# Optimization experiments

Measured on AMD Instinct MI355X. Metric: run time of the kernel, lower is better.

## Reference

```python
import jax, jax.numpy as jnp
import numpy as np

E, H, KVH, S, N = 2048, 16, 4, 4096, 1
D = E // H            # head_dim = 128
G = H // KVH          # groups = 4
KV_DIM = KVH * D


def setup_inputs() -> dict:
    key = jax.random.key(0)
    ks = jax.random.split(key, 7)
    sc = 0.02
    seq = jax.random.normal(ks[0], (N, S, E), dtype=jnp.float32)
    # causal mask, 0 = masked (matches masked_fill(mask == 0, -inf))
    mask = jnp.tril(jnp.ones((S, S), dtype=jnp.int32))[None, None]  # [1,1,S,S]
    return {
        "seq": seq,
        "mask": mask,
        "Wq_w": jax.random.normal(ks[1], (E, E), dtype=jnp.float32) * sc,
        "Wq_b": jnp.zeros((E,), dtype=jnp.float32),
        "Wkv_w": jax.random.normal(ks[2], (2 * KV_DIM, E), dtype=jnp.float32) * sc,
        "Wkv_b": jnp.zeros((2 * KV_DIM,), dtype=jnp.float32),
        "Wo_w": jax.random.normal(ks[3], (E, E), dtype=jnp.float32) * sc,
        "Wo_b": jnp.zeros((E,), dtype=jnp.float32),
    }


def reference(seq, mask, Wq_w, Wq_b, Wkv_w, Wkv_b, Wo_w, Wo_b):
    n, s, _ = seq.shape
    q = seq @ Wq_w.T + Wq_b                      # [N,S,E]
    kv = seq @ Wkv_w.T + Wkv_b                   # [N,S,2*KV_DIM]
    Q = q.reshape(n, s, H, D).transpose(0, 2, 1, 3)         # [N,H,S,D]
    KV = kv.reshape(n, s, 2, KVH, D)
    K = KV[:, :, 0].transpose(0, 2, 1, 3)                   # [N,KVH,S,D]
    V = KV[:, :, 1].transpose(0, 2, 1, 3)                   # [N,KVH,S,D]
    # repeat_interleave over head dim (GQA expansion)
    Kr = jnp.repeat(K, G, axis=1)                           # [N,H,S,D]
    Vr = jnp.repeat(V, G, axis=1)
    energy = jnp.einsum("nhqd,nhkd->nhqk", Q, Kr)           # [N,H,S,S]
    neg = jnp.finfo(energy.dtype).min
    energy = jnp.where(mask == 0, neg, energy)
    attn = jax.nn.softmax(energy / jnp.sqrt(jnp.float32(D)), axis=3)
    out = jnp.einsum("nhqk,nhkd->nhqd", attn, Vr)           # [N,H,S,D]
    out = out.transpose(0, 2, 1, 3).reshape(n, s, E)
    out = out @ Wo_w.T + Wo_b
    return out, K, V
```

## Files before the change

kernel.cpp:

```cpp
#include <hip/hip_runtime.h>
#include <cstdint>
#include <cstddef>

typedef __bf16 bf16_t;
typedef __bf16 bf16x4 __attribute__((ext_vector_type(4)));
typedef __bf16 bf16x8 __attribute__((ext_vector_type(8)));
typedef float  f32x4  __attribute__((ext_vector_type(4)));

#define LDQ 3072

__global__ __launch_bounds__(256)
void cast_kernel(const float* __restrict__ in, bf16_t* __restrict__ out, int n8) {
  int i = blockIdx.x * 256 + threadIdx.x;
  if (i >= n8) return;
  const float4* p = reinterpret_cast<const float4*>(in) + (size_t)i * 2;
  float4 a = p[0], b = p[1];
  bf16x8 o;
  o[0] = (bf16_t)a.x; o[1] = (bf16_t)a.y; o[2] = (bf16_t)a.z; o[3] = (bf16_t)a.w;
  o[4] = (bf16_t)b.x; o[5] = (bf16_t)b.y; o[6] = (bf16_t)b.z; o[7] = (bf16_t)b.w;
  *reinterpret_cast<bf16x8*>(out + (size_t)i * 8) = o;
}

template <int MODE>
__global__ __launch_bounds__(256)
void gemm_bt(const bf16_t* __restrict__ A, const bf16_t* __restrict__ B,
             const float* __restrict__ bias0, const float* __restrict__ bias1,
             void* __restrict__ out0, float* __restrict__ kvout,
             bf16_t* __restrict__ vt, int M, int N, int K) {
  __shared__ __align__(16) bf16_t As[128][64];
  __shared__ __align__(16) bf16_t Bs[128][64];
  const int t = threadIdx.x;
  const int l = t & 63, w = t >> 6;
  const int lr = l & 15, lh = l >> 4;
  const int m0 = blockIdx.x * 128, n0 = blockIdx.y * 128;
  const int wm = (w >> 1) * 64, wn = (w & 1) * 64;

  f32x4 acc[4][4] = {};

  for (int kt = 0; kt < K; kt += 64) {
    #pragma unroll
    for (int it = 0; it < 4; ++it) {
      int e = (it * 256 + t) * 8;
      int row = e >> 6, col = e & 63;
      __builtin_amdgcn_global_load_lds(
          (const __attribute__((address_space(1))) void*)(A + (size_t)(m0 + row) * K + kt + col),
          (__attribute__((address_space(3))) void*)(&As[row][col]), 16, 0, 0);
      __builtin_amdgcn_global_load_lds(
          (const __attribute__((address_space(1))) void*)(B + (size_t)(n0 + row) * K + kt + col),
          (__attribute__((address_space(3))) void*)(&Bs[row][col]), 16, 0, 0);
    }
    __syncthreads();
    #pragma unroll
    for (int ks = 0; ks < 2; ++ks) {
      bf16x8 a[4], b[4];
      #pragma unroll
      for (int i = 0; i < 4; ++i)
        a[i] = *reinterpret_cast<const bf16x8*>(&As[wm + i * 16 + lr][ks * 32 + lh * 8]);
      #pragma unroll
      for (int j = 0; j < 4; ++j)
        b[j] = *reinterpret_cast<const bf16x8*>(&Bs[wn + j * 16 + lr][ks * 32 + lh * 8]);
      #pragma unroll
      for (int i = 0; i < 4; ++i)
        #pragma unroll
        for (int j = 0; j < 4; ++j)
          acc[i][j] = __builtin_amdgcn_mfma_f32_16x16x32_bf16(a[i], b[j], acc[i][j], 0, 0, 0);
    }
    __syncthreads();
  }

  #pragma unroll
  for (int j = 0; j < 4; ++j) {
    const int col = n0 + wn + j * 16 + lr;
    float bv;
    if constexpr (MODE == 0) bv = bias0[col];
    else bv = (col < 2048) ? bias0[col] : bias1[col - 2048];
    #pragma unroll
    for (int i = 0; i < 4; ++i) {
      #pragma unroll
      for (int r = 0; r < 4; ++r) {
        const int row = m0 + wm + i * 16 + lh * 4 + r;
        float v = acc[i][j][r] + bv;
        if constexpr (MODE == 0) {
          reinterpret_cast<float*>(out0)[(size_t)row * N + col] = v;
        } else {
          float qv = (col < 2048) ? v * 0.1275187541f : v;
          reinterpret_cast<bf16_t*>(out0)[(size_t)row * N + col] = (bf16_t)qv;
          if (col >= 2048) {
            const int local = col - 2048;
            const int which = local >> 9;
            const int hd    = local & 511;
            kvout[(size_t)which * 2097152 +
                  ((size_t)(hd >> 7) * 4096 + row) * 128 + (hd & 127)] = v;
            if (local >= 512) {
              const int c2 = local - 512;
              vt[(size_t)(c2 >> 7) * 524288 + (size_t)(c2 & 127) * 4096 + row] = (bf16_t)v;
            }
          }
        }
      }
    }
  }
}

__global__ __launch_bounds__(512, 2)
void attn_kernel(const bf16_t* __restrict__ QKVb, const bf16_t* __restrict__ Vt,
                 bf16_t* __restrict__ Ob) {
  __shared__ __align__(16) char smem[65536];
  const int t = threadIdx.x;
  const int w = t >> 6, l = t & 63;
  const int lr = l & 15, lh = l >> 4;
  const int g = w >> 2;
  const int wq = w & 3;
  const int h = blockIdx.y, kvh = h >> 2;

  const char* Kg = (const char*)(QKVb + 2048 + (size_t)kvh * 128);
  const char* Vg = (const char*)(Vt + (size_t)kvh * 524288);

#define STAGE_K(buf, kv0)                                                          \
  {                                                                                \
    _Pragma("unroll")                                                              \
    for (int p = 0; p < 2; ++p) {                                                  \
      int chunk = p * 512 + t;                                                     \
      int row = chunk >> 4, cb = (chunk & 15) << 4;                                \
      __builtin_amdgcn_global_load_lds(                                            \
        (const __attribute__((address_space(1))) void*)                            \
            (Kg + (size_t)((kv0) + row) * 6144 + (cb ^ ((row & 7) << 4))),         \
        (__attribute__((address_space(3))) void*)(smem + (buf) * 16384 + chunk * 16),\
        16, 0, 0);                                                                 \
    }                                                                              \
  }
#define STAGE_V(buf, kv0)                                                          \
  {                                                                                \
    _Pragma("unroll")                                                              \
    for (int p = 0; p < 2; ++p) {                                                  \
      int chunk = p * 512 + t;                                                     \
      int row = chunk >> 3, cb = (chunk & 7) << 4;                                 \
      __builtin_amdgcn_global_load_lds(                                            \
        (const __attribute__((address_space(1))) void*)                            \
            (Vg + (size_t)row * 8192 + (size_t)(kv0) * 2 + (cb ^ ((row & 7) << 4))),\
        (__attribute__((address_space(3))) void*)(smem + 32768 + (buf) * 16384 + chunk * 16),\
        16, 0, 0);                                                                 \
    }                                                                              \
  }

  bf16x8 onesf;
  #pragma unroll
  for (int j = 0; j < 8; ++j) onesf[j] = (bf16_t)1.0f;

  for (int ph = 0; ph < 2; ++ph) {
    const int xt = ph ? 31 - (int)blockIdx.x : (int)blockIdx.x;
    const int q0b = xt * 128;
    const int q0w = q0b + wq * 32;
    const int nIter = 2 * xt + 2;

    bf16x8 qf[2][4];
    #pragma unroll
    for (int sub = 0; sub < 2; ++sub) {
      const bf16_t* qp = QKVb + (size_t)(q0w + sub * 16 + lr) * LDQ + h * 128 + lh * 8;
      #pragma unroll
      for (int kc = 0; kc < 4; ++kc) qf[sub][kc] = *reinterpret_cast<const bf16x8*>(qp + kc * 32);
    }
    __builtin_amdgcn_sched_barrier(0);
    STAGE_K(0, 0);
    STAGE_V(0, 0);
    __builtin_amdgcn_sched_barrier(0);
    STAGE_K(1, 64);
    STAGE_V(1, 64);
    __builtin_amdgcn_sched_barrier(0);

    f32x4 oacc[2][8] = {};
    f32x4 lacc[2] = {};

    auto body = [&](int it, bool masked) {
      const int cur = it & 1;
      const int kv0 = it * 64;
      if (it + 1 < nIter) { asm volatile("s_waitcnt vmcnt(4)" ::: "memory"); }
      else                { asm volatile("s_waitcnt vmcnt(0)" ::: "memory"); }
      __builtin_amdgcn_s_barrier();
      __builtin_amdgcn_sched_barrier(0);

      const char* kb = smem + cur * 16384;
      f32x4 s[2][2] = {};
      __builtin_amdgcn_s_setprio(1);
      #pragma unroll
      for (int n2 = 0; n2 < 2; ++n2) {
        const int row = g * 32 + n2 * 16 + lr;
        const int sw = (row & 7) << 4;
        #pragma unroll
        for (int kc = 0; kc < 4; ++kc) {
          bf16x8 kf = *reinterpret_cast<const bf16x8*>(kb + row * 256 + ((kc * 64 + lh * 16) ^ sw));
          s[0][n2] = __builtin_amdgcn_mfma_f32_16x16x32_bf16(kf, qf[0][kc], s[0][n2], 0, 0, 0);
          s[1][n2] = __builtin_amdgcn_mfma_f32_16x16x32_bf16(kf, qf[1][kc], s[1][n2], 0, 0, 0);
        }
      }
      __builtin_amdgcn_s_setprio(0);

      bf16x8 pa[2];
      #pragma unroll
      for (int sub = 0; sub < 2; ++sub) {
        const int qs = q0w + sub * 16;
        const bool needM = masked && (kv0 + g * 32 + 31 > qs);
        bf16x8 v;
        #pragma unroll
        for (int n2 = 0; n2 < 2; ++n2) {
          #pragma unroll
          for (int r = 0; r < 4; ++r) {
            float p = exp2f(s[sub][n2][r]);
            if (needM && (kv0 + g * 32 + n2 * 16 + lh * 4 + r > qs + lr)) p = 0.f;
            v[n2 * 4 + r] = (bf16_t)p;
          }
        }
        pa[sub] = v;
      }
      lacc[0] = __builtin_amdgcn_mfma_f32_16x16x32_bf16(pa[0], onesf, lacc[0], 0, 0, 0);
      lacc[1] = __builtin_amdgcn_mfma_f32_16x16x32_bf16(pa[1], onesf, lacc[1], 0, 0, 0);

      const char* vb0 = smem + 32768 + cur * 16384;
      __builtin_amdgcn_s_setprio(1);
      #pragma unroll
      for (int nb = 0; nb < 8; ++nb) {
        const int row = nb * 16 + lr;
        const int sw2 = (row & 7) << 4;
        const char* vb = vb0 + row * 128;
        bf16x4 lo = *reinterpret_cast<const bf16x4*>(vb + ((g * 64 + lh * 8) ^ sw2));
        bf16x4 hi = *reinterpret_cast<const bf16x4*>(vb + ((g * 64 + 32 + lh * 8) ^ sw2));
        bf16x8 vf = __builtin_shufflevector(lo, hi, 0, 1, 2, 3, 4, 5, 6, 7);
        oacc[0][nb] = __builtin_amdgcn_mfma_f32_16x16x32_bf16(pa[0], vf, oacc[0][nb], 0, 0, 0);
        oacc[1][nb] = __builtin_amdgcn_mfma_f32_16x16x32_bf16(pa[1], vf, oacc[1][nb], 0, 0, 0);
      }
      __builtin_amdgcn_s_setprio(0);

      __builtin_amdgcn_sched_barrier(0);
      __builtin_amdgcn_s_barrier();
      __builtin_amdgcn_sched_barrier(0);
      if (it + 2 < nIter) { STAGE_K(cur, kv0 + 128); STAGE_V(cur, kv0 + 128); }
    };

    for (int it = 0; it < nIter - 2; ++it) body(it, false);
    body(nIter - 2, true);
    body(nIter - 1, true);

    bf16_t* mO = (bf16_t*)smem;
    float*  mL = (float*)(smem + 32768);
    if (g == 1) {
      #pragma unroll
      for (int sub = 0; sub < 2; ++sub) {
        #pragma unroll
        for (int nb = 0; nb < 8; ++nb)
          #pragma unroll
          for (int r = 0; r < 4; ++r)
            mO[((wq * 32 + sub * 16 + lh * 4 + r) << 7) + nb * 16 + lr] = (bf16_t)oacc[sub][nb][r];
        if (lr == 0)
          #pragma unroll
          for (int r = 0; r < 4; ++r) mL[wq * 32 + sub * 16 + lh * 4 + r] = lacc[sub][r];
      }
    }
    __syncthreads();
    if (g == 0) {
      #pragma unroll
      for (int sub = 0; sub < 2; ++sub) {
        f32x4 linv;
        #pragma unroll
        for (int r = 0; r < 4; ++r)
          linv[r] = 1.0f / (lacc[sub][r] + mL[wq * 32 + sub * 16 + lh * 4 + r]);
        #pragma unroll
        for (int nb = 0; nb < 8; ++nb) {
          #pragma unroll
          for (int r = 0; r < 4; ++r) {
            float o1 = (float)mO[((wq * 32 + sub * 16 + lh * 4 + r) << 7) + nb * 16 + lr];
            float v = (oacc[sub][nb][r] + o1) * linv[r];
            Ob[(size_t)(q0w + sub * 16 + lh * 4 + r) * 2048 + h * 128 + nb * 16 + lr] = (bf16_t)v;
          }
        }
      }
    }
    __syncthreads();
  }
#undef STAGE_K
#undef STAGE_V
}

extern "C" void kernel_launch(void* const* d_in, const int* in_sizes, int n_in,
                              void* d_out, int out_size, void* d_ws, size_t ws_size,
                              hipStream_t stream) {
  const float* seq   = (const float*)d_in[0];
  const float* Wq_w  = (const float*)d_in[2];
  const float* Wq_b  = (const float*)d_in[3];
  const float* Wkv_w = (const float*)d_in[4];
  const float* Wkv_b = (const float*)d_in[5];
  const float* Wo_w  = (const float*)d_in[6];
  const float* Wo_b  = (const float*)d_in[7];

  float* out   = (float*)d_out;
  float* kvout = out + (size_t)4096 * 2048;

  char* ws = (char*)d_ws;
  bf16_t* seqb = (bf16_t*)ws;
  bf16_t* wqkv = (bf16_t*)(ws + 16777216);
  bf16_t* wob  = (bf16_t*)(ws + 29360128);
  bf16_t* qkvb = (bf16_t*)(ws + 37748736);
  bf16_t* vt   = (bf16_t*)(ws + 62914560);
  bf16_t* ob   = seqb;

  cast_kernel<<<4096, 256, 0, stream>>>(seq, seqb, 1048576);
  cast_kernel<<<2048, 256, 0, stream>>>(Wq_w, wqkv, 524288);
  cast_kernel<<<1024, 256, 0, stream>>>(Wkv_w, wqkv + 4194304, 262144);
  cast_kernel<<<2048, 256, 0, stream>>>(Wo_w, wob, 524288);

  gemm_bt<1><<<dim3(32, 24), 256, 0, stream>>>(seqb, wqkv, Wq_b, Wkv_b,
                                               qkvb, kvout, vt, 4096, 3072, 2048);
  attn_kernel<<<dim3(16, 16), 512, 0, stream>>>(qkvb, vt, ob);
  gemm_bt<0><<<dim3(32, 16), 256, 0, stream>>>(ob, wob, Wo_b, nullptr,
                                               out, nullptr, nullptr, 4096, 2048, 2048);
}
```

Baseline: 274.9 us.

## Rewrite GEMMs with 256x256 tiles, double-buffered swizzled LDS and async prefetch

Replaces the 128x128 single-buffered GEMM with a 256x256 tile kernel using 512 threads, a double-buffered 64KB LDS ring with XOR-swizzled layout, and explicit vmcnt waits so global-to-LDS loads for the next K-step overlap MFMA compute. The aim is to raise data reuse per tile, avoid LDS bank conflicts, and hide load latency. The larger tiles cut the grid to 192 and 128 blocks, which may leave many of the CUs idle and add register pressure.

```diff
diff --git a/kernel.cpp b/kernel.cpp
--- a/kernel.cpp
+++ b/kernel.cpp
@@ -22,63 +22,107 @@
 }
 
 template <int MODE>
-__global__ __launch_bounds__(256)
-void gemm_bt(const bf16_t* __restrict__ A, const bf16_t* __restrict__ B,
+__global__ __launch_bounds__(512, 2)
+void gemm256(const bf16_t* __restrict__ A, const bf16_t* __restrict__ B,
              const float* __restrict__ bias0, const float* __restrict__ bias1,
              void* __restrict__ out0, float* __restrict__ kvout,
              bf16_t* __restrict__ vt, int M, int N, int K) {
-  __shared__ __align__(16) bf16_t As[128][64];
-  __shared__ __align__(16) bf16_t Bs[128][64];
+  __shared__ __align__(16) char smem[65536];
   const int t = threadIdx.x;
-  const int l = t & 63, w = t >> 6;
+  const int l = t & 63;
   const int lr = l & 15, lh = l >> 4;
-  const int m0 = blockIdx.x * 128, n0 = blockIdx.y * 128;
-  const int wm = (w >> 1) * 64, wn = (w & 1) * 64;
-
-  f32x4 acc[4][4] = {};
-
-  for (int kt = 0; kt < K; kt += 64) {
-    #pragma unroll
-    for (int it = 0; it < 4; ++it) {
-      int e = (it * 256 + t) * 8;
-      int row = e >> 6, col = e & 63;
-      __builtin_amdgcn_global_load_lds(
-          (const __attribute__((address_space(1))) void*)(A + (size_t)(m0 + row) * K + kt + col),
-          (__attribute__((address_space(3))) void*)(&As[row][col]), 16, 0, 0);
-      __builtin_amdgcn_global_load_lds(
-          (const __attribute__((address_space(1))) void*)(B + (size_t)(n0 + row) * K + kt + col),
-          (__attribute__((address_space(3))) void*)(&Bs[row][col]), 16, 0, 0);
-    }
-    __syncthreads();
-    #pragma unroll
-    for (int ks = 0; ks < 2; ++ks) {
-      bf16x8 a[4], b[4];
-      #pragma unroll
-      for (int i = 0; i < 4; ++i)
-        a[i] = *reinterpret_cast<const bf16x8*>(&As[wm + i * 16 + lr][ks * 32 + lh * 8]);
+  const int w = t >> 6;
+  const int wm = w >> 2, wn = w & 3;
+  const int m0 = blockIdx.x * 256, n0 = blockIdx.y * 256;
+
+  const char* Ag = (const char*)(A + (size_t)m0 * K);
+  const char* Bg = (const char*)(B + (size_t)n0 * K);
+
+#define STAGE_T(buf, kt)                                                            \
+  {                                                                                 \
+    _Pragma("unroll")                                                               \
+    for (int p = 0; p < 2; ++p) {                                                   \
+      int c = p * 512 + t;                                                          \
+      int lrow = c >> 3, ls = (c & 7) ^ (lrow & 7);                                 \
+      int row = (lrow << 1) | (ls >> 2), c8 = ls & 3;                               \
+      __builtin_amdgcn_global_load_lds(                                             \
+        (const __attribute__((address_space(1))) void*)                             \
+            (Ag + (size_t)row * (K * 2) + (kt) * 2 + c8 * 16),                      \
+        (__attribute__((address_space(3))) void*)(smem + (buf) * 32768 + c * 16),   \
+        16, 0, 0);                                                                  \
+    }                                                                               \
+    _Pragma("unroll")                                                               \
+    for (int p = 0; p < 2; ++p) {                                                   \
+      int c = p * 512 + t;                                                          \
+      int lrow = c >> 3, ls = (c & 7) ^ (lrow & 7);                                 \
+      int row = (lrow << 1) | (ls >> 2), c8 = ls & 3;                               \
+      __builtin_amdgcn_global_load_lds(                                             \
+        (const __attribute__((address_space(1))) void*)                             \
+            (Bg + (size_t)row * (K * 2) + (kt) * 2 + c8 * 16),                      \
+        (__attribute__((address_space(3))) void*)(smem + (buf) * 32768 + 16384 + c * 16), \
+        16, 0, 0);                                                                  \
+    }                                                                               \
+  }
+
+  f32x4 acc[8][4] = {};
+  const int T = K >> 5;
+
+  STAGE_T(0, 0);
+  STAGE_T(1, 32);
+
+  for (int kt = 0; kt < T; ++kt) {
+    const int cur = kt & 1;
+    if (kt + 1 < T) { asm volatile("s_waitcnt vmcnt(4)" ::: "memory"); }
+    else            { asm volatile("s_waitcnt vmcnt(0)" ::: "memory"); }
+    __builtin_amdgcn_s_barrier();
+    __builtin_amdgcn_sched_barrier(0);
+
+    const char* ab = smem + cur * 32768;
+    const char* bb = ab + 16384;
+    bf16x8 a[8], b[4];
+    #pragma unroll
+    for (int i = 0; i < 8; ++i) {
+      const int row = wm * 128 + i * 16 + lr;
+      const int lrow = row >> 1;
+      const int slot = (((row & 1) << 2) | lh) ^ (lrow & 7);
+      a[i] = *reinterpret_cast<const bf16x8*>(ab + lrow * 128 + slot * 16);
+    }
+    #pragma unroll
+    for (int j = 0; j < 4; ++j) {
+      const int row = wn * 64 + j * 16 + lr;
+      const int lrow = row >> 1;
+      const int slot = (((row & 1) << 2) | lh) ^ (lrow & 7);
+      b[j] = *reinterpret_cast<const bf16x8*>(bb + lrow * 128 + slot * 16);
+    }
+    asm volatile("s_waitcnt lgkmcnt(0)" ::: "memory");
+    __builtin_amdgcn_sched_barrier(0);
+
+    __builtin_amdgcn_s_setprio(1);
+    #pragma unroll
+    for (int i = 0; i < 8; ++i)
       #pragma unroll
       for (int j = 0; j < 4; ++j)
-        b[j] = *reinterpret_cast<const bf16x8*>(&Bs[wn + j * 16 + lr][ks * 32 + lh * 8]);
-      #pragma unroll
-      for (int i = 0; i < 4; ++i)
-        #pragma unroll
-        for (int j = 0; j < 4; ++j)
-          acc[i][j] = __builtin_amdgcn_mfma_f32_16x16x32_bf16(a[i], b[j], acc[i][j], 0, 0, 0);
-    }
-    __syncthreads();
-  }
+        acc[i][j] = __builtin_amdgcn_mfma_f32_16x16x32_bf16(a[i], b[j], acc[i][j], 0, 0, 0);
+    __builtin_amdgcn_s_setprio(0);
+
+    __builtin_amdgcn_sched_barrier(0);
+    __builtin_amdgcn_s_barrier();
+    __builtin_amdgcn_sched_barrier(0);
+    if (kt + 2 < T) STAGE_T(cur, (kt + 2) * 32);
+  }
+#undef STAGE_T
 
   #pragma unroll
   for (int j = 0; j < 4; ++j) {
-    const int col = n0 + wn + j * 16 + lr;
+    const int col = n0 + wn * 64 + j * 16 + lr;
     float bv;
     if constexpr (MODE == 0) bv = bias0[col];
     else bv = (col < 2048) ? bias0[col] : bias1[col - 2048];
     #pragma unroll
-    for (int i = 0; i < 4; ++i) {
+    for (int i = 0; i < 8; ++i) {
       #pragma unroll
       for (int r = 0; r < 4; ++r) {
-        const int row = m0 + wm + i * 16 + lh * 4 + r;
+        const int row = m0 + wm * 128 + i * 16 + lh * 4 + r;
         float v = acc[i][j][r] + bv;
         if constexpr (MODE == 0) {
           reinterpret_cast<float*>(out0)[(size_t)row * N + col] = v;
@@ -307,9 +351,9 @@
   cast_kernel<<<1024, 256, 0, stream>>>(Wkv_w, wqkv + 4194304, 262144);
   cast_kernel<<<2048, 256, 0, stream>>>(Wo_w, wob, 524288);
 
-  gemm_bt<1><<<dim3(32, 24), 256, 0, stream>>>(seqb, wqkv, Wq_b, Wkv_b,
+  gemm256<1><<<dim3(16, 12), 512, 0, stream>>>(seqb, wqkv, Wq_b, Wkv_b,
                                                qkvb, kvout, vt, 4096, 3072, 2048);
   attn_kernel<<<dim3(16, 16), 512, 0, stream>>>(qkvb, vt, ob);
-  gemm_bt<0><<<dim3(32, 16), 256, 0, stream>>>(ob, wob, Wo_b, nullptr,
-                                               out, nullptr, nullptr, 4096, 2048, 2048);
+  gemm256<0><<<dim3(16, 8), 512, 0, stream>>>(ob, wob, Wo_b, nullptr,
+                                              out, nullptr, nullptr, 4096, 2048, 2048);
 }
```

New measurement: 277.1 us. Within noise of the previous version (+0.8%).

## Replace GEMM with 256x256 tiled double-buffered swizzled LDS pipeline

Applied to the files above, without the earlier changes.

Swaps the 128x128 single-buffered GEMM for a 256x256 tile kernel with 512 threads. It double-buffers K-slices of 32 in LDS using direct global-to-LDS loads, applies an XOR swizzle to avoid bank conflicts, and interleaves loads with MFMA phases, raising MFMA priority around them. The aim is to hide global memory latency and get more reuse per tile. In exchange the grid shrinks (192 and 128 blocks on a many-CU part), which risks underfilling the device, and register pressure rises with 32 accumulators per thread.

```diff
diff --git a/kernel.cpp b/kernel.cpp
--- a/kernel.cpp
+++ b/kernel.cpp
@@ -22,63 +22,115 @@
 }
 
 template <int MODE>
-__global__ __launch_bounds__(256)
-void gemm_bt(const bf16_t* __restrict__ A, const bf16_t* __restrict__ B,
+__global__ __launch_bounds__(512, 2)
+void gemm256(const bf16_t* __restrict__ A, const bf16_t* __restrict__ B,
              const float* __restrict__ bias0, const float* __restrict__ bias1,
              void* __restrict__ out0, float* __restrict__ kvout,
              bf16_t* __restrict__ vt, int M, int N, int K) {
-  __shared__ __align__(16) bf16_t As[128][64];
-  __shared__ __align__(16) bf16_t Bs[128][64];
+  __shared__ __align__(16) char smem[65536];
   const int t = threadIdx.x;
-  const int l = t & 63, w = t >> 6;
+  const int l = t & 63;
   const int lr = l & 15, lh = l >> 4;
-  const int m0 = blockIdx.x * 128, n0 = blockIdx.y * 128;
-  const int wm = (w >> 1) * 64, wn = (w & 1) * 64;
-
-  f32x4 acc[4][4] = {};
-
-  for (int kt = 0; kt < K; kt += 64) {
-    #pragma unroll
-    for (int it = 0; it < 4; ++it) {
-      int e = (it * 256 + t) * 8;
-      int row = e >> 6, col = e & 63;
-      __builtin_amdgcn_global_load_lds(
-          (const __attribute__((address_space(1))) void*)(A + (size_t)(m0 + row) * K + kt + col),
-          (__attribute__((address_space(3))) void*)(&As[row][col]), 16, 0, 0);
-      __builtin_amdgcn_global_load_lds(
-          (const __attribute__((address_space(1))) void*)(B + (size_t)(n0 + row) * K + kt + col),
-          (__attribute__((address_space(3))) void*)(&Bs[row][col]), 16, 0, 0);
-    }
-    __syncthreads();
-    #pragma unroll
-    for (int ks = 0; ks < 2; ++ks) {
-      bf16x8 a[4], b[4];
-      #pragma unroll
-      for (int i = 0; i < 4; ++i)
-        a[i] = *reinterpret_cast<const bf16x8*>(&As[wm + i * 16 + lr][ks * 32 + lh * 8]);
-      #pragma unroll
-      for (int j = 0; j < 4; ++j)
-        b[j] = *reinterpret_cast<const bf16x8*>(&Bs[wn + j * 16 + lr][ks * 32 + lh * 8]);
-      #pragma unroll
-      for (int i = 0; i < 4; ++i)
-        #pragma unroll
-        for (int j = 0; j < 4; ++j)
-          acc[i][j] = __builtin_amdgcn_mfma_f32_16x16x32_bf16(a[i], b[j], acc[i][j], 0, 0, 0);
-    }
-    __syncthreads();
-  }
+  const int w = t >> 6;
+  const int wm = w >> 2, wn = w & 3;
+  const int m0 = blockIdx.x * 256, n0 = blockIdx.y * 256;
+
+  const char* Ag = (const char*)(A + (size_t)m0 * K);
+  const char* Bg = (const char*)(B + (size_t)n0 * K);
+
+#define STAGE_U(dst, src, ks)                                                   \
+  { _Pragma("unroll")                                                           \
+    for (int p = 0; p < 2; ++p) {                                               \
+      int c = p * 512 + t;                                                      \
+      int row = c >> 2;                                                         \
+      int c16 = (c & 3) ^ ((row >> 1) & 3);                                     \
+      __builtin_amdgcn_global_load_lds(                                         \
+        (const __attribute__((address_space(1))) void*)                         \
+          ((src) + (size_t)row * (size_t)(K * 2) + (size_t)(ks) * 64 + c16 * 16), \
+        (__attribute__((address_space(3))) void*)((dst) + c * 16), 16, 0, 0);   \
+    } }
+
+  f32x4 acc[8][4] = {};
+  bf16x8 a[4], b[4];
+  char* const s0 = smem;
+  char* const s1 = smem + 32768;
+
+#define RD_B(base)                                                              \
+  { _Pragma("unroll")                                                           \
+    for (int j = 0; j < 4; ++j) {                                               \
+      int row = wn * 64 + j * 16 + lr;                                          \
+      b[j] = *reinterpret_cast<const bf16x8*>(                                  \
+          (base) + 16384 + row * 64 + ((lh ^ ((row >> 1) & 3)) << 4));          \
+    } }
+#define RD_A(base, iq)                                                          \
+  { _Pragma("unroll")                                                           \
+    for (int i = 0; i < 4; ++i) {                                               \
+      int row = wm * 128 + (iq) * 64 + i * 16 + lr;                             \
+      a[i] = *reinterpret_cast<const bf16x8*>(                                  \
+          (base) + row * 64 + ((lh ^ ((row >> 1) & 3)) << 4));                  \
+    } }
+#define MFMA16(iq)                                                              \
+  asm volatile("s_waitcnt lgkmcnt(0)" ::: "memory");                            \
+  __builtin_amdgcn_sched_barrier(0);                                            \
+  __builtin_amdgcn_s_setprio(1);                                                \
+  { _Pragma("unroll")                                                           \
+    for (int i = 0; i < 4; ++i)                                                 \
+      _Pragma("unroll")                                                         \
+      for (int j = 0; j < 4; ++j)                                               \
+        acc[(iq) * 4 + i][j] =                                                  \
+          __builtin_amdgcn_mfma_f32_16x16x32_bf16(a[i], b[j], acc[(iq)*4+i][j], 0, 0, 0); } \
+  __builtin_amdgcn_s_setprio(0);                                                \
+  __builtin_amdgcn_sched_barrier(0);
+#define BAR  __builtin_amdgcn_s_barrier(); __builtin_amdgcn_sched_barrier(0);
+
+  const int NK = K >> 5;
+  STAGE_U(s0, Ag, 0);
+  STAGE_U(s0 + 16384, Bg, 0);
+
+  for (int it2 = 0; it2 < (NK >> 1); ++it2) {
+    const int k1 = 2 * it2 + 1, k2 = 2 * it2 + 2;
+    STAGE_U(s1, Ag, k1);
+    asm volatile("s_waitcnt vmcnt(2)" ::: "memory");
+    BAR;
+    RD_B(s0); RD_A(s0, 0);
+    MFMA16(0);
+    BAR;
+    RD_A(s0, 1);
+    STAGE_U(s1 + 16384, Bg, k1);
+    MFMA16(1);
+    BAR;
+    if (k2 < NK) {
+      STAGE_U(s0, Ag, k2);
+      asm volatile("s_waitcnt vmcnt(2)" ::: "memory");
+    } else {
+      asm volatile("s_waitcnt vmcnt(0)" ::: "memory");
+    }
+    BAR;
+    RD_B(s1); RD_A(s1, 0);
+    MFMA16(0);
+    BAR;
+    RD_A(s1, 1);
+    if (k2 < NK) STAGE_U(s0 + 16384, Bg, k2);
+    MFMA16(1);
+    BAR;
+  }
+#undef STAGE_U
+#undef RD_A
+#undef RD_B
+#undef MFMA16
+#undef BAR
 
   #pragma unroll
   for (int j = 0; j < 4; ++j) {
-    const int col = n0 + wn + j * 16 + lr;
+    const int col = n0 + wn * 64 + j * 16 + lr;
     float bv;
     if constexpr (MODE == 0) bv = bias0[col];
     else bv = (col < 2048) ? bias0[col] : bias1[col - 2048];
     #pragma unroll
-    for (int i = 0; i < 4; ++i) {
+    for (int i = 0; i < 8; ++i) {
       #pragma unroll
       for (int r = 0; r < 4; ++r) {
-        const int row = m0 + wm + i * 16 + lh * 4 + r;
+        const int row = m0 + wm * 128 + i * 16 + lh * 4 + r;
         float v = acc[i][j][r] + bv;
         if constexpr (MODE == 0) {
           reinterpret_cast<float*>(out0)[(size_t)row * N + col] = v;
@@ -307,9 +359,9 @@
   cast_kernel<<<1024, 256, 0, stream>>>(Wkv_w, wqkv + 4194304, 262144);
   cast_kernel<<<2048, 256, 0, stream>>>(Wo_w, wob, 524288);
 
-  gemm_bt<1><<<dim3(32, 24), 256, 0, stream>>>(seqb, wqkv, Wq_b, Wkv_b,
+  gemm256<1><<<dim3(16, 12), 512, 0, stream>>>(seqb, wqkv, Wq_b, Wkv_b,
                                                qkvb, kvout, vt, 4096, 3072, 2048);
   attn_kernel<<<dim3(16, 16), 512, 0, stream>>>(qkvb, vt, ob);
-  gemm_bt<0><<<dim3(32, 16), 256, 0, stream>>>(ob, wob, Wo_b, nullptr,
-                                               out, nullptr, nullptr, 4096, 2048, 2048);
+  gemm256<0><<<dim3(16, 8), 512, 0, stream>>>(ob, wob, Wo_b, nullptr,
+                                              out, nullptr, nullptr, 4096, 2048, 2048);
 }
```

Result: faster. 266.3 us (-3.1%).
